# Optimization experiments

Hardware: AMD Instinct MI355X
Metric: run time of the kernel (lower is better)

The kernel has to match this reference:

```python
import jax, jax.numpy as jnp
from jax import lax
import numpy as np

B, T, F, H, L, HOR = 512, 512, 16, 256, 3, 24


def setup_inputs() -> dict:
    key = jax.random.key(0)
    ks = jax.random.split(key, 9)
    s = 0.05
    x = jax.random.normal(ks[0], (B, T, F), dtype=jnp.float32)
    # PyTorch LSTM params: gate order (i, f, g, o), W_ih [4H, in], W_hh [4H, H]
    W_ih0 = jax.random.normal(ks[1], (4 * H, F), dtype=jnp.float32) * s
    W_ih12 = jax.random.normal(ks[2], (L - 1, 4 * H, H), dtype=jnp.float32) * s
    W_hh = jax.random.normal(ks[3], (L, 4 * H, H), dtype=jnp.float32) * s
    b_ih = jax.random.normal(ks[4], (L, 4 * H), dtype=jnp.float32) * s
    b_hh = jax.random.normal(ks[5], (L, 4 * H), dtype=jnp.float32) * s
    fc_W = jax.random.normal(ks[6], (HOR, H), dtype=jnp.float32) * s
    fc_b = jax.random.normal(ks[7], (HOR,), dtype=jnp.float32) * s
    return {"x": x, "W_ih0": W_ih0, "W_ih12": W_ih12, "W_hh": W_hh,
            "b_ih": b_ih, "b_hh": b_hh, "fc_W": fc_W, "fc_b": fc_b}


def _lstm_layer(x, W_ih, W_hh, b_ih, b_hh):
    # x: [B, T, in] -> h sequence [B, T, H]
    Bn = x.shape[0]
    Hn = W_hh.shape[1]
    # precompute input contribution for all timesteps (one big GEMM)
    xg = jnp.einsum('bti,gi->btg', x, W_ih) + b_ih  # [B, T, 4H]
    W_hh_T = W_hh.T  # [H, 4H]

    def step(carry, xg_t):
        h, c = carry
        gates = xg_t + h @ W_hh_T + b_hh  # [B, 4H]
        i, f, g, o = jnp.split(gates, 4, axis=-1)
        c = jax.nn.sigmoid(f) * c + jax.nn.sigmoid(i) * jnp.tanh(g)
        h = jax.nn.sigmoid(o) * jnp.tanh(c)
        return (h, c), h

    h0 = jnp.zeros((Bn, Hn), x.dtype)
    c0 = jnp.zeros((Bn, Hn), x.dtype)
    _, hs = lax.scan(step, (h0, c0), jnp.swapaxes(xg, 0, 1))  # [T, B, H]
    return jnp.swapaxes(hs, 0, 1)


def reference(x, W_ih0, W_ih12, W_hh, b_ih, b_hh, fc_W, fc_b):
    h = _lstm_layer(x, W_ih0, W_hh[0], b_ih[0], b_hh[0])
    for l in range(1, L):
        h = _lstm_layer(h, W_ih12[l - 1], W_hh[l], b_ih[l], b_hh[l])
    last_hidden = h[:, -1, :]  # [B, H]
    return last_hidden @ fc_W.T + fc_b  # [B, horizon]
```

## Files before the change

kernel.cpp:

```cpp
#include <hip/hip_runtime.h>
#include <hip/hip_bf16.h>
#include <stdint.h>

#define Bsz 512
#define Tsz 512
#define Fsz 16
#define Hsz 256
#define HORZ 24

#define NG 8
#define NBT 8
#define BT 64
#define USL 32
#define PD 8
#define HBUF_ELEMS ((size_t)3*PD*Bsz*Hsz)
#define NFLAGS (3*NG*NBT)
#define AROW_B 512
#define ABUF_B (BT*AROW_B)
#define HTILE_B (BT*64)
#define SMEM_B (3*ABUF_B + HTILE_B)

#define POISON   0x7FC07FC0u
#define POISON64 0x7FC07FC07FC07FC0ull

typedef float  f32x4  __attribute__((ext_vector_type(4)));
typedef float  f32x16 __attribute__((ext_vector_type(16)));
typedef __bf16 bf16x8 __attribute__((ext_vector_type(8)));
typedef uint32_t u32x2 __attribute__((ext_vector_type(2)));
typedef uint32_t u32x4 __attribute__((ext_vector_type(4)));

__device__ __forceinline__ float sigm(float v){ return 1.f/(1.f+__expf(-v)); }

__device__ __forceinline__ bf16x8 ld_sc01_b128(const void* p){
  bf16x8 r;
  asm volatile("global_load_dwordx4 %0, %1, off sc0 sc1" : "=&v"(r) : "v"(p) : "memory");
  return r;
}
__device__ __forceinline__ u32x2 ld_b64_async(const void* p){
  u32x2 r;
  asm volatile("global_load_dwordx2 %0, %1, off" : "=&v"(r) : "v"(p) : "memory");
  return r;
}
__device__ __forceinline__ void st_sc01_b64(void* p, uint64_t v){
  asm volatile("global_store_dwordx2 %0, %1, off sc0 sc1" :: "v"(p), "v"(v) : "memory");
}
__device__ __forceinline__ void st_sc01_b32(void* p, uint32_t v){
  asm volatile("global_store_dword %0, %1, off sc0 sc1" :: "v"(p), "v"(v) : "memory");
}
__device__ __forceinline__ uint32_t ld_sc01_b32(const void* p){
  uint32_t r;
  asm volatile("global_load_dword %0, %1, off sc0 sc1\n\ts_waitcnt vmcnt(0)"
    : "=&v"(r) : "v"(p) : "memory");
  return r;
}
__device__ __forceinline__ void wait_flag(const unsigned int* fp, int target){
  int guard = 0;
  while ((int)ld_sc01_b32(fp) < target){
    __builtin_amdgcn_s_sleep(1);
    if (++guard > (1<<18)) break;
  }
}
__device__ __forceinline__ bool poison_free(const bf16x8* v){
  bool ok = true;
  #pragma unroll
  for (int j=0;j<4;++j){
    u32x4 uv = __builtin_bit_cast(u32x4, v[j]);
    ok = ok && (uv[0] != POISON) && (uv[2] != POISON);
  }
  return ok;
}
__device__ __forceinline__ void poll_load4(bf16x8* dst, const __bf16* src){
  int guard = 0;
  for(;;){
    #pragma unroll
    for (int j=0;j<4;++j) dst[j] = ld_sc01_b128(src + j*8);
    asm volatile("s_waitcnt vmcnt(0)" ::: "memory");
    __builtin_amdgcn_sched_barrier(0);
    if (poison_free(dst)) break;
    __builtin_amdgcn_s_sleep(4);
    if (++guard > (1<<16)) break;
  }
}

template<bool L0>
__device__ __forceinline__ void lstm_body(
    int l, int g, int nb, int tid,
    const float* __restrict__ xin,
    const float* __restrict__ Wih0,
    const float* __restrict__ Wih12,
    const float* __restrict__ Whh,
    const float* __restrict__ bih,
    const float* __restrict__ bhh,
    __bf16* __restrict__ hb,
    unsigned int* __restrict__ flags,
    char* smem)
{
  char* ain0  = smem;
  char* ain1  = smem + ABUF_B;
  char* hrc   = smem + 2*ABUF_B;
  char* htile = smem + 3*ABUF_B;

  const int lane = tid & 63;
  const int wid  = tid >> 6;
  const int wm   = wid >> 2;
  const int wn   = wid & 3;
  const int b0   = nb * BT;
  const int m0   = wm * 32;
  const int n0   = wn * 32;

  const int colL = n0 + (lane & 31);
  const int hi   = lane >> 5;
  const int kg8  = hi * 8;
  const int kg16 = hi * 16;
  const int R    = (colL&3)*Hsz + g*USL + (colL>>2);
  const float bias = bih[l*4*Hsz + R] + bhh[l*4*Hsz + R];
  const int rowA = m0 + (lane & 31);
  const int swzA = (rowA & 7) << 4;

  constexpr int NC = L0 ? 17 : 32;
  bf16x8 w[NC];
  {
    const float* recB = Whh + ((size_t)l*4*Hsz + R)*Hsz;
    #pragma unroll
    for (int c=0;c<NC;++c){
      const float* p;
      if constexpr (L0) p = (c==0) ? (Wih0 + (size_t)R*Fsz + kg8)
                                   : (recB + (c-1)*16 + kg8);
      else              p = (c<16) ? (Wih12 + ((size_t)(l-1)*4*Hsz + R)*Hsz + c*16 + kg8)
                                   : (recB + (c-16)*16 + kg8);
      f32x4 u0 = *(const f32x4*)p;
      f32x4 u1 = *(const f32x4*)(p+4);
      bf16x8 t;
      #pragma unroll
      for (int j=0;j<4;++j){ t[j]=(__bf16)u0[j]; t[j+4]=(__bf16)u1[j]; }
      w[c] = t;
    }
  }

  const int srow = tid >> 3, sq = tid & 7;
  const int sswz = (srow & 7) << 4;
  const size_t sgrow = (size_t)(b0 + srow) * Hsz;

  float cst[16];
  #pragma unroll
  for (int i=0;i<16;++i) cst[i]=0.f;

  unsigned int* myflag = flags + ((l*NG+g)*NBT + nb);
  const bool q2 = ((colL & 3) == 2);
  auto slotp = [&](int ll, int s){ return hb + ((size_t)ll*PD + (s&(PD-1)))*Bsz*Hsz; };

  {
    u32x4 z = {0,0,0,0};
    #pragma unroll
    for (int j=0;j<4;++j) *(u32x4*)(hrc + tid*64 + j*16) = z;
  }
  if constexpr (L0){
    u32x2 xv = ld_b64_async(xin + ((size_t)(b0+srow)*Tsz + 0)*Fsz + sq*2);
    asm volatile("s_waitcnt vmcnt(0)" ::: "memory");
    __builtin_amdgcn_sched_barrier(0);
    char* d = ain0 + srow*32 + sq*4;
    *(__bf16*)(d)   = (__bf16)__uint_as_float(xv[0]);
    *(__bf16*)(d+2) = (__bf16)__uint_as_float(xv[1]);
  } else {
    bf16x8 av[4];
    poll_load4(av, slotp(l-1,0) + sgrow + sq*32);
    #pragma unroll
    for (int j=0;j<4;++j)
      *(bf16x8*)(ain0 + srow*AROW_B + ((sq*64 + j*16) ^ sswz)) = av[j];
  }
  __syncthreads();

  for (int t=0; t<Tsz; ++t){
    if (l < 2 && (t & 3) == 0){
      if (tid < 8 && t >= 4)
        wait_flag(flags + (((l+1)*NG + tid)*NBT + nb), t-3);
      __syncthreads();
    }

    char* aprd = (t&1) ? ain1 : ain0;
    char* apwr = (t&1) ? ain0 : ain1;
    bf16x8 hiv[4];
    const __bf16* pfsrc = nullptr;
    const bool pfon = (!L0) && (t+1 < Tsz);

    if constexpr (L0){
      u32x2 xv = ld_b64_async(xin + ((size_t)(b0+srow)*Tsz + t)*Fsz + sq*2);
      bf16x8 hrv[4];
      if (t > 0) poll_load4(hrv, slotp(l,t-1) + sgrow + sq*32);
      else { asm volatile("s_waitcnt vmcnt(0)" ::: "memory");
             __builtin_amdgcn_sched_barrier(0); }
      char* d = ain0 + srow*32 + sq*4;
      *(__bf16*)(d)   = (__bf16)__uint_as_float(xv[0]);
      *(__bf16*)(d+2) = (__bf16)__uint_as_float(xv[1]);
      if (t > 0){
        #pragma unroll
        for (int j=0;j<4;++j)
          *(bf16x8*)(hrc + srow*AROW_B + ((sq*64 + j*16) ^ sswz)) = hrv[j];
      }
      __syncthreads();
    } else {
      if (t > 0){
        bf16x8 hrv[4];
        poll_load4(hrv, slotp(l,t-1) + sgrow + sq*32);
        #pragma unroll
        for (int j=0;j<4;++j)
          *(bf16x8*)(hrc + srow*AROW_B + ((sq*64 + j*16) ^ sswz)) = hrv[j];
      }
      if (pfon){
        pfsrc = slotp(l-1,t+1) + sgrow + sq*32;
        #pragma unroll
        for (int j=0;j<4;++j) hiv[j] = ld_sc01_b128(pfsrc + j*8);
      }
      __syncthreads();
    }

    f32x16 acc;
    #pragma unroll
    for (int i=0;i<16;++i) acc[i]=0.f;
    #pragma unroll
    for (int c=0;c<NC;++c){
      bf16x8 af;
      if constexpr (L0){
        if (c==0) af = *(const bf16x8*)(ain0 + rowA*32 + kg16);
        else      af = *(const bf16x8*)(hrc + rowA*AROW_B + ((((c-1)*32) + kg16) ^ swzA));
      } else {
        if (c<16) af = *(const bf16x8*)(aprd + rowA*AROW_B + (((c*32) + kg16) ^ swzA));
        else      af = *(const bf16x8*)(hrc  + rowA*AROW_B + ((((c-16)*32) + kg16) ^ swzA));
      }
      acc = __builtin_amdgcn_mfma_f32_32x32x16_bf16(af, w[c], acc, 0,0,0);
    }

    #pragma unroll
    for (int i=0;i<16;++i){
      float v  = acc[i] + bias;
      float vv = q2 ? 2.f*v : v;
      float sg = sigm(vv);
      float act = q2 ? (2.f*sg - 1.f) : sg;
      float a1 = __shfl_xor(act,1,64);
      float a2 = __shfl_xor(act,2,64);
      float a3 = __shfl_xor(act,3,64);
      if ((lane&3)==0){
        float cn = a1*cst[i] + act*a2;
        cst[i] = cn;
        float th = 2.f*sigm(2.f*cn) - 1.f;
        float hv = a3*th;
        int r = (i&3) + 8*(i>>2) + 4*hi;
        int unit = colL >> 2;
        *(__bf16*)(htile + (m0 + r)*64 + unit*2) = (__bf16)hv;
      }
    }
    __syncthreads();

    {
      uint64_t v = *(const uint64_t*)(htile + srow*64 + sq*8);
      st_sc01_b64(slotp(l,t)   + sgrow + g*USL + sq*4, v);
      st_sc01_b64(slotp(l,t+2) + sgrow + g*USL + sq*4, POISON64);
    }
    asm volatile("s_waitcnt vmcnt(0)" ::: "memory");
    __builtin_amdgcn_sched_barrier(0);
    if (pfon){
      if (!poison_free(hiv)) poll_load4(hiv, pfsrc);
      #pragma unroll
      for (int j=0;j<4;++j)
        *(bf16x8*)(apwr + srow*AROW_B + ((sq*64 + j*16) ^ sswz)) = hiv[j];
    }
    __syncthreads();
    if (tid==0) st_sc01_b32(myflag, (uint32_t)(t+1));
  }
}

__global__ __launch_bounds__(512, 2) void lstm_persist(
    const float* __restrict__ xin,
    const float* __restrict__ Wih0,
    const float* __restrict__ Wih12,
    const float* __restrict__ Whh,
    const float* __restrict__ bih,
    const float* __restrict__ bhh,
    __bf16* __restrict__ hb,
    unsigned int* __restrict__ flags)
{
  __shared__ __align__(16) char smem[SMEM_B];
  const int bid = blockIdx.x;
  const int l   = bid >> 6;
  const int g   = (bid >> 3) & 7;
  const int nb  = bid & 7;
  const int tid = threadIdx.x;
  if (l == 0)
    lstm_body<true >(l,g,nb,tid, xin,Wih0,Wih12,Whh,bih,bhh, hb,flags, smem);
  else
    lstm_body<false>(l,g,nb,tid, xin,Wih0,Wih12,Whh,bih,bhh, hb,flags, smem);
}

__global__ void init_ws(uint32_t* __restrict__ hb32, uint32_t* __restrict__ flags)
{
  size_t i = (size_t)blockIdx.x*blockDim.x + threadIdx.x;
  size_t n = (HBUF_ELEMS*2)/16;
  if (i < n){
    u32x4 v = {POISON, POISON, POISON, POISON};
    *(u32x4*)(hb32 + i*4) = v;
  }
  if (i < NFLAGS) flags[i] = 0;
}

__global__ void fc_kernel(const __bf16* __restrict__ hb,
                          const float* __restrict__ fcW,
                          const float* __restrict__ fcb,
                          float* __restrict__ out)
{
  __shared__ float hs[Hsz];
  int b = blockIdx.x;
  const __bf16* hp = hb + ((size_t)(2*PD + ((Tsz-1)&(PD-1))))*Bsz*Hsz + (size_t)b*Hsz;
  for (int i = threadIdx.x; i < Hsz; i += 64) hs[i] = (float)hp[i];
  __syncthreads();
  int o = threadIdx.x;
  if (o < HORZ) {
    float a = fcb[o];
    #pragma unroll 8
    for (int u=0; u<Hsz; ++u) a += hs[u]*fcW[o*Hsz + u];
    out[b*HORZ + o] = a;
  }
}

extern "C" void kernel_launch(void* const* d_in, const int* in_sizes, int n_in,
                              void* d_out, int out_size, void* d_ws, size_t ws_size,
                              hipStream_t stream)
{
  const float* x     = (const float*)d_in[0];
  const float* Wih0  = (const float*)d_in[1];
  const float* Wih12 = (const float*)d_in[2];
  const float* Whh   = (const float*)d_in[3];
  const float* bih   = (const float*)d_in[4];
  const float* bhh   = (const float*)d_in[5];
  const float* fcW   = (const float*)d_in[6];
  const float* fcb   = (const float*)d_in[7];

  __bf16* hb = (__bf16*)d_ws;
  unsigned int* flags = (unsigned int*)((char*)d_ws + HBUF_ELEMS*2);

  size_t nchunk = (HBUF_ELEMS*2)/16;
  int ib = (int)((nchunk + 255) / 256);
  hipLaunchKernelGGL(init_ws, dim3(ib), dim3(256), 0, stream, (uint32_t*)hb, flags);

  hipLaunchKernelGGL(lstm_persist, dim3(3*NG*NBT), dim3(512), 0, stream,
                     x, Wih0, Wih12, Whh, bih, bhh, hb, flags);
  hipLaunchKernelGGL(fc_kernel, dim3(Bsz), dim3(64), 0, stream, hb, fcW, fcb, (float*)d_out);
}
```

Measured before the change: 3.195 ms.

## Overlap recurrent h-load latency with input-projection MFMAs in LSTM step

Restructures each timestep so the input-contribution MFMAs (layer input or x) run from a double-buffered LDS tile while the previous-step hidden state is loaded from global memory. Only afterwards does it check for poison, store h to LDS, sync, and run the recurrent MFMAs. Layer 0 now prefetches x for t+1 into the alternate buffer, like the upper layers already do. It also shortens the spin-wait sleep. The risks are more register pressure and a changed buffer ordering for layer 0, which needs the initial x fill to match.

```diff
diff --git a/kernel.cpp b/kernel.cpp
--- a/kernel.cpp
+++ b/kernel.cpp
@@ -77,7 +77,7 @@
     asm volatile("s_waitcnt vmcnt(0)" ::: "memory");
     __builtin_amdgcn_sched_barrier(0);
     if (poison_free(dst)) break;
-    __builtin_amdgcn_s_sleep(4);
+    __builtin_amdgcn_s_sleep(1);
     if (++guard > (1<<16)) break;
   }
 }
@@ -118,6 +118,7 @@
   const int swzA = (rowA & 7) << 4;
 
   constexpr int NC = L0 ? 17 : 32;
+  constexpr int NH = L0 ? 1  : 16;
   bf16x8 w[NC];
   {
     const float* recB = Whh + ((size_t)l*4*Hsz + R)*Hsz;
@@ -179,54 +180,51 @@
 
     char* aprd = (t&1) ? ain1 : ain0;
     char* apwr = (t&1) ? ain0 : ain1;
-    bf16x8 hiv[4];
-    const __bf16* pfsrc = nullptr;
-    const bool pfon = (!L0) && (t+1 < Tsz);
-
-    if constexpr (L0){
-      u32x2 xv = ld_b64_async(xin + ((size_t)(b0+srow)*Tsz + t)*Fsz + sq*2);
-      bf16x8 hrv[4];
-      if (t > 0) poll_load4(hrv, slotp(l,t-1) + sgrow + sq*32);
-      else { asm volatile("s_waitcnt vmcnt(0)" ::: "memory");
-             __builtin_amdgcn_sched_barrier(0); }
-      char* d = ain0 + srow*32 + sq*4;
-      *(__bf16*)(d)   = (__bf16)__uint_as_float(xv[0]);
-      *(__bf16*)(d+2) = (__bf16)__uint_as_float(xv[1]);
-      if (t > 0){
-        #pragma unroll
-        for (int j=0;j<4;++j)
-          *(bf16x8*)(hrc + srow*AROW_B + ((sq*64 + j*16) ^ sswz)) = hrv[j];
-      }
-      __syncthreads();
-    } else {
-      if (t > 0){
-        bf16x8 hrv[4];
-        poll_load4(hrv, slotp(l,t-1) + sgrow + sq*32);
-        #pragma unroll
-        for (int j=0;j<4;++j)
-          *(bf16x8*)(hrc + srow*AROW_B + ((sq*64 + j*16) ^ sswz)) = hrv[j];
-      }
-      if (pfon){
+
+    bf16x8 hrv[4];
+    const __bf16* hrsrc = slotp(l,t-1) + sgrow + sq*32;
+    if (t > 0){
+      #pragma unroll
+      for (int j=0;j<4;++j) hrv[j] = ld_sc01_b128(hrsrc + j*8);
+    }
+    __builtin_amdgcn_sched_barrier(0);
+
+    f32x16 acc;
+    #pragma unroll
+    for (int i=0;i<16;++i) acc[i]=0.f;
+    #pragma unroll
+    for (int c=0;c<NH;++c){
+      bf16x8 af;
+      if constexpr (L0) af = *(const bf16x8*)(aprd + rowA*32 + kg16);
+      else              af = *(const bf16x8*)(aprd + rowA*AROW_B + (((c*32) + kg16) ^ swzA));
+      acc = __builtin_amdgcn_mfma_f32_32x32x16_bf16(af, w[c], acc, 0,0,0);
+    }
+    __builtin_amdgcn_sched_barrier(0);
+
+    if (t > 0){
+      asm volatile("s_waitcnt vmcnt(0)" ::: "memory");
+      __builtin_amdgcn_sched_barrier(0);
+      if (!poison_free(hrv)) poll_load4(hrv, hrsrc);
+      #pragma unroll
+      for (int j=0;j<4;++j)
+        *(bf16x8*)(hrc + srow*AROW_B + ((sq*64 + j*16) ^ sswz)) = hrv[j];
+    }
+    bf16x8 hiv[4]; u32x2 xv; const __bf16* pfsrc = nullptr;
+    const bool pfon = (t+1 < Tsz);
+    if (pfon){
+      if constexpr (L0){
+        xv = ld_b64_async(xin + ((size_t)(b0+srow)*Tsz + (t+1))*Fsz + sq*2);
+      } else {
         pfsrc = slotp(l-1,t+1) + sgrow + sq*32;
         #pragma unroll
         for (int j=0;j<4;++j) hiv[j] = ld_sc01_b128(pfsrc + j*8);
       }
-      __syncthreads();
-    }
-
-    f32x16 acc;
-    #pragma unroll
-    for (int i=0;i<16;++i) acc[i]=0.f;
-    #pragma unroll
-    for (int c=0;c<NC;++c){
-      bf16x8 af;
-      if constexpr (L0){
-        if (c==0) af = *(const bf16x8*)(ain0 + rowA*32 + kg16);
-        else      af = *(const bf16x8*)(hrc + rowA*AROW_B + ((((c-1)*32) + kg16) ^ swzA));
-      } else {
-        if (c<16) af = *(const bf16x8*)(aprd + rowA*AROW_B + (((c*32) + kg16) ^ swzA));
-        else      af = *(const bf16x8*)(hrc  + rowA*AROW_B + ((((c-16)*32) + kg16) ^ swzA));
-      }
+    }
+    __syncthreads();
+
+    #pragma unroll
+    for (int c=NH;c<NC;++c){
+      bf16x8 af = *(const bf16x8*)(hrc + rowA*AROW_B + ((((c-NH)*32) + kg16) ^ swzA));
       acc = __builtin_amdgcn_mfma_f32_32x32x16_bf16(af, w[c], acc, 0,0,0);
     }
 
@@ -259,10 +257,16 @@
     asm volatile("s_waitcnt vmcnt(0)" ::: "memory");
     __builtin_amdgcn_sched_barrier(0);
     if (pfon){
-      if (!poison_free(hiv)) poll_load4(hiv, pfsrc);
-      #pragma unroll
-      for (int j=0;j<4;++j)
-        *(bf16x8*)(apwr + srow*AROW_B + ((sq*64 + j*16) ^ sswz)) = hiv[j];
+      if constexpr (L0){
+        char* d = apwr + srow*32 + sq*4;
+        *(__bf16*)(d)   = (__bf16)__uint_as_float(xv[0]);
+        *(__bf16*)(d+2) = (__bf16)__uint_as_float(xv[1]);
+      } else {
+        if (!poison_free(hiv)) poll_load4(hiv, pfsrc);
+        #pragma unroll
+        for (int j=0;j<4;++j)
+          *(bf16x8*)(apwr + srow*AROW_B + ((sq*64 + j*16) ^ sswz)) = hiv[j];
+      }
     }
     __syncthreads();
     if (tid==0) st_sc01_b32(myflag, (uint32_t)(t+1));
```

Result: slower. 3.315 ms (+3.8%).
